# Optimization experiments

Hardware: AMD Instinct MI355X
Metric: run time of the kernel (lower is better)

## Reference

```python
import jax, jax.numpy as jnp
import numpy as np

K = 1.0        # Lorentz manifold curvature parameter
EPS = 1e-7     # arccosh argument clamp (geoopt float32 eps)


def projx(x):
    # Project onto the hyperboloid: x0 = sqrt(K + ||x_1:||^2)
    rest = x[..., 1:]
    x0 = jnp.sqrt(K + jnp.sum(rest * rest, axis=-1, keepdims=True))
    return jnp.concatenate([x0, rest], axis=-1)


def setup_inputs() -> dict:
    key = jax.random.key(0)
    k1, k2 = jax.random.split(key)
    B, C, D = 16384, 2048, 512
    x = jax.random.normal(k1, (B, D), dtype=jnp.float32)
    # ManifoldParameter: random_normal with std = 1/sqrt(n_dim)
    points = jax.random.normal(k2, (C, D), dtype=jnp.float32) * (1.0 / np.sqrt(D))
    return {"x": x, "points": points}


def reference(x, points):
    xp = projx(x)        # (B, D) on hyperboloid
    pp = projx(points)   # (C, D) on hyperboloid
    # Minkowski inner <x,p>_L = -x0*p0 + sum_{i>0} x_i p_i = x.p - 2*x0*p0
    # Computed as a GEMM plus a rank-1 correction (avoids (B,C,D) intermediate).
    inner = xp @ pp.T - 2.0 * jnp.outer(xp[:, 0], pp[:, 0])  # (B, C)
    d = jnp.sqrt(K) * jnp.arccosh(jnp.maximum(-inner / K, 1.0 + EPS))
    return -d  # (B, C) negative Riemannian distances (class logits)
```

## Files before the change

kernel.cpp:

```cpp
#include <hip/hip_runtime.h>
#include <hip/hip_bf16.h>
#include <stdint.h>

#define B_ROWS 16384
#define C_ROWS 2048
#define D_FULL 512
#define KP     512

#define BM 128
#define BN 128
#define BK 64

typedef __attribute__((ext_vector_type(8))) short bf16x8;
typedef __attribute__((ext_vector_type(4))) float f32x4;

typedef __attribute__((address_space(1))) void glb_void;
typedef __attribute__((address_space(3))) void lds_void;

__device__ __forceinline__ void gld16(const void* g, void* l) {
    __builtin_amdgcn_global_load_lds((glb_void*)(uintptr_t)g,
                                     (lds_void*)(uintptr_t)l, 16, 0, 0);
}

__global__ __launch_bounds__(256) void prep_kernel(
    const float* __restrict__ x, const float* __restrict__ pts,
    unsigned short* __restrict__ Abf, unsigned short* __restrict__ Bbf,
    float* __restrict__ xn, float* __restrict__ pn)
{
    int row = blockIdx.x;
    const float* src;
    unsigned short* dst;
    float* nrm;
    if (row < B_ROWS) {
        src = x + (size_t)row * D_FULL;
        dst = Abf + (size_t)row * KP;
        nrm = xn + row;
    } else {
        int r = row - B_ROWS;
        src = pts + (size_t)r * D_FULL;
        dst = Bbf + (size_t)r * KP;
        nrm = pn + r;
    }
    int t = threadIdx.x;
    float v0 = src[t + 1];
    float v1 = (t < 255) ? src[t + 257] : 0.0f;
    __hip_bfloat16 b0 = __float2bfloat16(v0);
    __hip_bfloat16 b1 = __float2bfloat16(v1);
    dst[t]       = *(unsigned short*)&b0;
    dst[t + 256] = *(unsigned short*)&b1;
    float ss = v0 * v0 + v1 * v1;
    #pragma unroll
    for (int off = 32; off > 0; off >>= 1) ss += __shfl_down(ss, off);
    __shared__ float red[4];
    if ((t & 63) == 0) red[t >> 6] = ss;
    __syncthreads();
    if (t == 0) nrm[0] = sqrtf(1.0f + red[0] + red[1] + red[2] + red[3]);
}

__global__ __launch_bounds__(256) void gemm_kernel(
    const unsigned short* __restrict__ A,
    const unsigned short* __restrict__ Bm,
    const float* __restrict__ xn, const float* __restrict__ pn,
    float* __restrict__ out)
{
    __shared__ unsigned short As[BM * BK];
    __shared__ unsigned short Bs[BN * BK];

    const int tid  = threadIdx.x;
    const int wave = tid >> 6;
    const int lane = tid & 63;
    const int wm   = wave >> 1;
    const int wn   = wave & 1;
    const int lrow = lane & 15;
    const int quad = lane >> 4;

    const int bm0 = blockIdx.x * BM;
    const int bn0 = blockIdx.y * BN;

    const int srow = wave * 32 + (lane >> 3);
    const int scol = (((lane & 7) ^ ((lane >> 3) & 7)) << 3);

    const unsigned short* gA = A  + (size_t)(bm0 + srow) * KP + scol;
    const unsigned short* gB = Bm + (size_t)(bn0 + srow) * KP + scol;

    f32x4 acc[4][4] = {};

    for (int k0 = 0; k0 < KP; k0 += BK) {
        __syncthreads();
        #pragma unroll
        for (int i = 0; i < 4; ++i) {
            gld16(gA + (size_t)(i * 8) * KP + k0, &As[(wave * 32 + i * 8) * BK]);
            gld16(gB + (size_t)(i * 8) * KP + k0, &Bs[(wave * 32 + i * 8) * BK]);
        }
        __syncthreads();

        #pragma unroll
        for (int kk = 0; kk < BK; kk += 32) {
            const int ch0 = kk >> 3;
            bf16x8 af[4], bfr[4];
            #pragma unroll
            for (int mi = 0; mi < 4; ++mi) {
                int r = wm * 64 + mi * 16 + lrow;
                af[mi] = *(const bf16x8*)&As[r * BK + (((ch0 + quad) ^ (lrow & 7)) << 3)];
            }
            #pragma unroll
            for (int ni = 0; ni < 4; ++ni) {
                int r = wn * 64 + ni * 16 + lrow;
                bfr[ni] = *(const bf16x8*)&Bs[r * BK + (((ch0 + quad) ^ (lrow & 7)) << 3)];
            }
            #pragma unroll
            for (int mi = 0; mi < 4; ++mi)
                #pragma unroll
                for (int ni = 0; ni < 4; ++ni)
                    acc[mi][ni] = __builtin_amdgcn_mfma_f32_16x16x32_bf16(
                        af[mi], bfr[ni], acc[mi][ni], 0, 0, 0);
        }
    }

    float pv[4];
    #pragma unroll
    for (int ni = 0; ni < 4; ++ni)
        pv[ni] = pn[bn0 + wn * 64 + ni * 16 + lrow];

    #pragma unroll
    for (int mi = 0; mi < 4; ++mi) {
        #pragma unroll
        for (int r = 0; r < 4; ++r) {
            int row = bm0 + wm * 64 + mi * 16 + quad * 4 + r;
            float xv = xn[row];
            size_t base = (size_t)row * C_ROWS + bn0 + wn * 64 + lrow;
            #pragma unroll
            for (int ni = 0; ni < 4; ++ni) {
                float z = fmaf(xv, pv[ni], -acc[mi][ni][r]);
                z = fmaxf(z, 1.0f + 1e-7f);
                out[base + ni * 16] = -__logf(z + __fsqrt_rn(z * z - 1.0f));
            }
        }
    }
}

extern "C" void kernel_launch(void* const* d_in, const int* in_sizes, int n_in,
                              void* d_out, int out_size, void* d_ws, size_t ws_size,
                              hipStream_t stream) {
    const float* x   = (const float*)d_in[0];
    const float* pts = (const float*)d_in[1];
    float* out = (float*)d_out;

    char* ws = (char*)d_ws;
    unsigned short* Abf = (unsigned short*)ws;
    unsigned short* Bbf = (unsigned short*)(ws + (size_t)B_ROWS * KP * 2);
    float* xn = (float*)(ws + (size_t)(B_ROWS + C_ROWS) * KP * 2);
    float* pn = (float*)((char*)xn + (size_t)B_ROWS * 4);
    (void)in_sizes; (void)n_in; (void)out_size; (void)ws_size;

    prep_kernel<<<B_ROWS + C_ROWS, 256, 0, stream>>>(x, pts, Abf, Bbf, xn, pn);

    dim3 grid(B_ROWS / BM, C_ROWS / BN);
    gemm_kernel<<<grid, 256, 0, stream>>>(Abf, Bbf, xn, pn, out);
}
```

Before: 199.3 us.

## Double-buffer GEMM LDS tiles and pack bf16 pairs in prep kernel

The GEMM main loop now uses two LDS buffers for the A and B tiles. Global-to-LDS loads for the next K tile are issued before computing on the current one, which removes one barrier per iteration and lets load latency overlap with the MFMA work. This doubles LDS use per block and adds a launch-bounds occupancy hint of 2 blocks per CU. The prep kernel also has each thread convert adjacent element pairs and write them as a single 32-bit packed store.

Measured after the change: 196.1 us. No clear change (-1.6%).

```diff
diff --git a/kernel.cpp b/kernel.cpp
--- a/kernel.cpp
+++ b/kernel.cpp
@@ -42,12 +42,14 @@
         nrm = pn + r;
     }
     int t = threadIdx.x;
-    float v0 = src[t + 1];
-    float v1 = (t < 255) ? src[t + 257] : 0.0f;
+    float v0 = src[2 * t + 1];
+    float v1 = (t < 255) ? src[2 * t + 2] : 0.0f;
     __hip_bfloat16 b0 = __float2bfloat16(v0);
     __hip_bfloat16 b1 = __float2bfloat16(v1);
-    dst[t]       = *(unsigned short*)&b0;
-    dst[t + 256] = *(unsigned short*)&b1;
+    union { unsigned short u[2]; unsigned int w; } pack;
+    pack.u[0] = *(unsigned short*)&b0;
+    pack.u[1] = *(unsigned short*)&b1;
+    *(unsigned int*)&dst[2 * t] = pack.w;
     float ss = v0 * v0 + v1 * v1;
     #pragma unroll
     for (int off = 32; off > 0; off >>= 1) ss += __shfl_down(ss, off);
@@ -57,14 +59,14 @@
     if (t == 0) nrm[0] = sqrtf(1.0f + red[0] + red[1] + red[2] + red[3]);
 }
 
-__global__ __launch_bounds__(256) void gemm_kernel(
+__global__ __launch_bounds__(256, 2) void gemm_kernel(
     const unsigned short* __restrict__ A,
     const unsigned short* __restrict__ Bm,
     const float* __restrict__ xn, const float* __restrict__ pn,
     float* __restrict__ out)
 {
-    __shared__ unsigned short As[BM * BK];
-    __shared__ unsigned short Bs[BN * BK];
+    __shared__ unsigned short As[2][BM * BK];
+    __shared__ unsigned short Bs[2][BN * BK];
 
     const int tid  = threadIdx.x;
     const int wave = tid >> 6;
@@ -85,15 +87,24 @@
 
     f32x4 acc[4][4] = {};
 
-    for (int k0 = 0; k0 < KP; k0 += BK) {
+    #pragma unroll
+    for (int i = 0; i < 4; ++i) {
+        gld16(gA + (size_t)(i * 8) * KP, &As[0][(wave * 32 + i * 8) * BK]);
+        gld16(gB + (size_t)(i * 8) * KP, &Bs[0][(wave * 32 + i * 8) * BK]);
+    }
+
+    #pragma unroll 2
+    for (int it = 0; it < KP / BK; ++it) {
+        const int buf = it & 1;
         __syncthreads();
-        #pragma unroll
-        for (int i = 0; i < 4; ++i) {
-            gld16(gA + (size_t)(i * 8) * KP + k0, &As[(wave * 32 + i * 8) * BK]);
-            gld16(gB + (size_t)(i * 8) * KP + k0, &Bs[(wave * 32 + i * 8) * BK]);
+        if (it + 1 < KP / BK) {
+            const int k1 = (it + 1) * BK;
+            #pragma unroll
+            for (int i = 0; i < 4; ++i) {
+                gld16(gA + (size_t)(i * 8) * KP + k1, &As[buf ^ 1][(wave * 32 + i * 8) * BK]);
+                gld16(gB + (size_t)(i * 8) * KP + k1, &Bs[buf ^ 1][(wave * 32 + i * 8) * BK]);
+            }
         }
-        __syncthreads();
-
         #pragma unroll
         for (int kk = 0; kk < BK; kk += 32) {
             const int ch0 = kk >> 3;
@@ -101,12 +112,12 @@
             #pragma unroll
             for (int mi = 0; mi < 4; ++mi) {
                 int r = wm * 64 + mi * 16 + lrow;
-                af[mi] = *(const bf16x8*)&As[r * BK + (((ch0 + quad) ^ (lrow & 7)) << 3)];
+                af[mi] = *(const bf16x8*)&As[buf][r * BK + (((ch0 + quad) ^ (lrow & 7)) << 3)];
             }
             #pragma unroll
             for (int ni = 0; ni < 4; ++ni) {
                 int r = wn * 64 + ni * 16 + lrow;
-                bfr[ni] = *(const bf16x8*)&Bs[r * BK + (((ch0 + quad) ^ (lrow & 7)) << 3)];
+                bfr[ni] = *(const bf16x8*)&Bs[buf][r * BK + (((ch0 + quad) ^ (lrow & 7)) << 3)];
             }
             #pragma unroll
             for (int mi = 0; mi < 4; ++mi)
```
